# Kernel optimization log

Measured on AMD Instinct MI355X. Metric: run time of the kernel, lower is better.

The kernel has to match this reference:

```python
import jax, jax.numpy as jnp
import numpy as np

N = 4096
IN_DIM = 6
HID = 32
HEADS1 = 4
OUT_DIM = 64


def _gat_layer(x, mask, W, a_src, a_dst, b):
    # x: [n, in], W: [in, heads*d], a_src/a_dst: [heads, d], b: [heads*d]
    n = x.shape[0]
    heads, d = a_src.shape
    h = (x @ W).reshape(n, heads, d)                      # [n, heads, d]
    e_src = jnp.einsum('nhd,hd->nh', h, a_src)            # [n, heads]
    e_dst = jnp.einsum('nhd,hd->nh', h, a_dst)            # [n, heads]
    logits = e_src[:, None, :] + e_dst[None, :, :]        # [n, n, heads]
    logits = jax.nn.leaky_relu(logits, negative_slope=0.2)
    logits = jnp.where(mask[:, :, None], logits, jnp.float32(-1e9))
    alpha = jax.nn.softmax(logits, axis=1)                # softmax over j (dim=1)
    # dropout disabled (eval mode reference)
    out = jnp.einsum('ijh,jhd->ihd', alpha, h).reshape(n, heads * d)
    return out + b


def setup_inputs() -> dict:
    key = jax.random.key(0)
    ks = jax.random.split(key, 10)
    x = jax.random.normal(ks[0], (N, IN_DIM), dtype=jnp.float32)
    adj = jax.random.bernoulli(ks[1], 0.01, (N, N)).astype(jnp.float32)
    s = 0.1
    W1 = jax.random.normal(ks[2], (IN_DIM, HEADS1 * HID), dtype=jnp.float32) * s
    a_src1 = jax.random.normal(ks[3], (HEADS1, HID), dtype=jnp.float32) * s
    a_dst1 = jax.random.normal(ks[4], (HEADS1, HID), dtype=jnp.float32) * s
    b1 = jnp.zeros((HEADS1 * HID,), dtype=jnp.float32)
    W2 = jax.random.normal(ks[5], (HEADS1 * HID, OUT_DIM), dtype=jnp.float32) * s
    a_src2 = jax.random.normal(ks[6], (1, OUT_DIM), dtype=jnp.float32) * s
    a_dst2 = jax.random.normal(ks[7], (1, OUT_DIM), dtype=jnp.float32) * s
    b2 = jnp.zeros((OUT_DIM,), dtype=jnp.float32)
    return {'x': x, 'adj': adj, 'W1': W1, 'a_src1': a_src1, 'a_dst1': a_dst1,
            'b1': b1, 'W2': W2, 'a_src2': a_src2, 'a_dst2': a_dst2, 'b2': b2}


def reference(x, adj, W1, a_src1, a_dst1, b1, W2, a_src2, a_dst2, b2):
    n = x.shape[0]
    # add self loops: a = max(a, I), mask = a > 0
    a = jnp.maximum(adj, jnp.eye(n, dtype=adj.dtype))
    mask = a > 0
    h1 = jax.nn.elu(_gat_layer(x, mask, W1, a_src1, a_dst1, b1))
    # dropout disabled (eval mode)
    h2 = _gat_layer(h1, mask, W2, a_src2, a_dst2, b2)
    return h2
```

## Files before the change

kernel.cpp:

```cpp
#include <hip/hip_runtime.h>
#include <hip/hip_bf16.h>

#define N 4096
#define IN_DIM 6
#define HID 32
#define HEADS1 4
#define D1 (HEADS1*HID)
#define OUT_DIM 64
#define MAXNB 192

__global__ void k1_h1pre(const float* __restrict__ x,
                         const float* __restrict__ W1,
                         const float* __restrict__ a_src1,
                         const float* __restrict__ a_dst1,
                         float* __restrict__ hpre,
                         float* __restrict__ es1,
                         float* __restrict__ ed1) {
    int i = blockIdx.x;
    int t = threadIdx.x;
    __shared__ float xs[IN_DIM];
    if (t < IN_DIM) xs[t] = x[i*IN_DIM + t];
    __syncthreads();
    float acc = 0.f;
    #pragma unroll
    for (int k = 0; k < IN_DIM; ++k)
        acc += xs[k] * W1[k*D1 + t];
    hpre[(size_t)i*D1 + t] = acc;
    float ps = acc * a_src1[t];
    float pd = acc * a_dst1[t];
    #pragma unroll
    for (int off = 16; off >= 1; off >>= 1) {
        ps += __shfl_xor(ps, off, 64);
        pd += __shfl_xor(pd, off, 64);
    }
    if ((t & 31) == 0) {
        int h = t >> 5;
        es1[i*HEADS1 + h] = ps;
        ed1[i*HEADS1 + h] = pd;
    }
}

__global__ void k2_csr(const float* __restrict__ adj,
                       int* __restrict__ cnt, int* __restrict__ idxg) {
    int i = blockIdx.x;
    int t = threadIdx.x;
    __shared__ int c;
    __shared__ int list[MAXNB];
    if (t == 0) c = 0;
    __syncthreads();
    const float4* row = (const float4*)(adj + (size_t)i * N);
    for (int k = t; k < N/4; k += 256) {
        float4 v = row[k];
        float f[4] = {v.x, v.y, v.z, v.w};
        #pragma unroll
        for (int q = 0; q < 4; ++q) {
            int j = k*4 + q;
            if (f[q] > 0.f || j == i) {
                int p = atomicAdd(&c, 1);
                if (p < MAXNB) list[p] = j;
            }
        }
    }
    __syncthreads();
    int cc = min(c, MAXNB);
    if (t == 0) cnt[i] = cc;
    for (int p = t; p < cc; p += 256) idxg[i*MAXNB + p] = list[p];
}

__global__ void k3_agg1(const float* __restrict__ hpre,
                        const float* __restrict__ es1,
                        const float* __restrict__ ed1,
                        const int* __restrict__ cnt,
                        const int* __restrict__ idxg,
                        const float* __restrict__ b1,
                        float* __restrict__ h1) {
    int i = blockIdx.x;
    int t = threadIdx.x;
    int c = cnt[i];
    __shared__ int js[MAXNB];
    __shared__ float alpha[HEADS1][MAXNB];
    __shared__ float esi[HEADS1];
    if (t < HEADS1) esi[t] = es1[i*HEADS1 + t];
    for (int p = t; p < c; p += 128) js[p] = idxg[i*MAXNB + p];
    __syncthreads();
    for (int p = t; p < c; p += 128) {
        int j = js[p];
        #pragma unroll
        for (int h = 0; h < HEADS1; ++h) {
            float l = esi[h] + ed1[j*HEADS1 + h];
            alpha[h][p] = (l > 0.f) ? l : 0.2f*l;
        }
    }
    __syncthreads();
    int h = t >> 5, lane = t & 31;
    float m = -1e30f;
    for (int p = lane; p < c; p += 32) m = fmaxf(m, alpha[h][p]);
    #pragma unroll
    for (int off = 16; off >= 1; off >>= 1) m = fmaxf(m, __shfl_xor(m, off, 64));
    float s = 0.f;
    for (int p = lane; p < c; p += 32) s += __expf(alpha[h][p] - m);
    #pragma unroll
    for (int off = 16; off >= 1; off >>= 1) s += __shfl_xor(s, off, 64);
    float inv = 1.f / s;
    for (int p = lane; p < c; p += 32) alpha[h][p] = __expf(alpha[h][p] - m) * inv;
    __syncthreads();
    float acc = 0.f;
    for (int p = 0; p < c; ++p)
        acc += alpha[h][p] * hpre[(size_t)js[p]*D1 + t];
    acc += b1[t];
    h1[(size_t)i*D1 + t] = (acc > 0.f) ? acc : expm1f(acc);
}

__global__ void k4_h2pre(const float* __restrict__ h1,
                         const float* __restrict__ W2,
                         const float* __restrict__ a_src2,
                         const float* __restrict__ a_dst2,
                         float* __restrict__ h2pre,
                         float* __restrict__ es2,
                         float* __restrict__ ed2) {
    int i = blockIdx.x;
    int t = threadIdx.x;
    __shared__ float hs[D1];
    hs[t]      = h1[(size_t)i*D1 + t];
    hs[t + 64] = h1[(size_t)i*D1 + t + 64];
    __syncthreads();
    float acc = 0.f;
    #pragma unroll
    for (int k = 0; k < D1; ++k)
        acc += hs[k] * W2[k*OUT_DIM + t];
    h2pre[(size_t)i*OUT_DIM + t] = acc;
    float ps = acc * a_src2[t];
    float pd = acc * a_dst2[t];
    #pragma unroll
    for (int off = 32; off >= 1; off >>= 1) {
        ps += __shfl_xor(ps, off, 64);
        pd += __shfl_xor(pd, off, 64);
    }
    if (t == 0) { es2[i] = ps; ed2[i] = pd; }
}

__global__ void k5_agg2(const float* __restrict__ h2pre,
                        const float* __restrict__ es2,
                        const float* __restrict__ ed2,
                        const int* __restrict__ cnt,
                        const int* __restrict__ idxg,
                        const float* __restrict__ b2v,
                        float* __restrict__ out) {
    int i = blockIdx.x;
    int t = threadIdx.x;
    int c = cnt[i];
    __shared__ int js[MAXNB];
    __shared__ float alpha[MAXNB];
    for (int p = t; p < c; p += 64) js[p] = idxg[i*MAXNB + p];
    __syncthreads();
    float esi = es2[i];
    float m = -1e30f;
    for (int p = t; p < c; p += 64) {
        float l = esi + ed2[js[p]];
        l = (l > 0.f) ? l : 0.2f*l;
        alpha[p] = l;
        m = fmaxf(m, l);
    }
    #pragma unroll
    for (int off = 32; off >= 1; off >>= 1) m = fmaxf(m, __shfl_xor(m, off, 64));
    __syncthreads();
    float s = 0.f;
    for (int p = t; p < c; p += 64) s += __expf(alpha[p] - m);
    #pragma unroll
    for (int off = 32; off >= 1; off >>= 1) s += __shfl_xor(s, off, 64);
    float inv = 1.f / s;
    for (int p = t; p < c; p += 64) alpha[p] = __expf(alpha[p] - m) * inv;
    __syncthreads();
    float acc = 0.f;
    for (int p = 0; p < c; ++p)
        acc += alpha[p] * h2pre[(size_t)js[p]*OUT_DIM + t];
    acc += b2v[t];
    out[(size_t)i*OUT_DIM + t] = acc;
}

extern "C" void kernel_launch(void* const* d_in, const int* in_sizes, int n_in,
                              void* d_out, int out_size, void* d_ws, size_t ws_size,
                              hipStream_t stream) {
    const float* x      = (const float*)d_in[0];
    const float* adj    = (const float*)d_in[1];
    const float* W1     = (const float*)d_in[2];
    const float* a_src1 = (const float*)d_in[3];
    const float* a_dst1 = (const float*)d_in[4];
    const float* b1     = (const float*)d_in[5];
    const float* W2     = (const float*)d_in[6];
    const float* a_src2 = (const float*)d_in[7];
    const float* a_dst2 = (const float*)d_in[8];
    const float* b2v    = (const float*)d_in[9];
    float* out = (float*)d_out;

    float* ws    = (float*)d_ws;
    float* hpre  = ws;
    float* h1    = hpre  + (size_t)N*D1;
    float* h2pre = h1    + (size_t)N*D1;
    float* es1   = h2pre + (size_t)N*OUT_DIM;
    float* ed1   = es1   + (size_t)N*HEADS1;
    float* es2   = ed1   + (size_t)N*HEADS1;
    float* ed2   = es2   + N;
    int*   cnt   = (int*)(ed2 + N);
    int*   idxg  = cnt + N;

    k1_h1pre<<<N, 128, 0, stream>>>(x, W1, a_src1, a_dst1, hpre, es1, ed1);
    k2_csr  <<<N, 256, 0, stream>>>(adj, cnt, idxg);
    k3_agg1 <<<N, 128, 0, stream>>>(hpre, es1, ed1, cnt, idxg, b1, h1);
    k4_h2pre<<<N,  64, 0, stream>>>(h1, W2, a_src2, a_dst2, h2pre, es2, ed2);
    k5_agg2 <<<N,  64, 0, stream>>>(h2pre, es2, ed2, cnt, idxg, b2v, out);
}
```

Before: 136.5 us.

## Fuse CSR build, layer-1 aggregation and layer-2 projection into one kernel

Merges the adjacency scan, the layer-1 attention softmax and aggregation, and the h1·W2 projection into a single per-row kernel, cutting five launches to three. Logits are computed at the point where each neighbour is discovered, h1 never goes to global memory, and the aggregation is split across two thread groups. Softmax normalisation is deferred to after aggregation in both layers, which removes a second exp pass. kA now handles two rows per block. The cost is higher shared-memory use and more register pressure in the fused kernel, which can lower occupancy.

```diff
diff --git a/kernel.cpp b/kernel.cpp
--- a/kernel.cpp
+++ b/kernel.cpp
@@ -1,5 +1,4 @@
 #include <hip/hip_runtime.h>
-#include <hip/hip_bf16.h>
 
 #define N 4096
 #define IN_DIM 6
@@ -9,46 +8,66 @@
 #define OUT_DIM 64
 #define MAXNB 192
 
-__global__ void k1_h1pre(const float* __restrict__ x,
-                         const float* __restrict__ W1,
-                         const float* __restrict__ a_src1,
-                         const float* __restrict__ a_dst1,
-                         float* __restrict__ hpre,
-                         float* __restrict__ es1,
-                         float* __restrict__ ed1) {
-    int i = blockIdx.x;
-    int t = threadIdx.x;
-    __shared__ float xs[IN_DIM];
-    if (t < IN_DIM) xs[t] = x[i*IN_DIM + t];
+__global__ void kA(const float* __restrict__ x,
+                   const float* __restrict__ W1,
+                   const float* __restrict__ a_src1,
+                   const float* __restrict__ a_dst1,
+                   float* __restrict__ hpre,
+                   float* __restrict__ es1,
+                   float* __restrict__ ed1) {
+    int t  = threadIdx.x;
+    int r  = t >> 7;
+    int tt = t & 127;
+    int i  = blockIdx.x * 2 + r;
+    __shared__ float xs[2][IN_DIM];
+    if (tt < IN_DIM) xs[r][tt] = x[i*IN_DIM + tt];
     __syncthreads();
     float acc = 0.f;
     #pragma unroll
     for (int k = 0; k < IN_DIM; ++k)
-        acc += xs[k] * W1[k*D1 + t];
-    hpre[(size_t)i*D1 + t] = acc;
-    float ps = acc * a_src1[t];
-    float pd = acc * a_dst1[t];
+        acc += xs[r][k] * W1[k*D1 + tt];
+    hpre[(size_t)i*D1 + tt] = acc;
+    float ps = acc * a_src1[tt];
+    float pd = acc * a_dst1[tt];
     #pragma unroll
     for (int off = 16; off >= 1; off >>= 1) {
         ps += __shfl_xor(ps, off, 64);
         pd += __shfl_xor(pd, off, 64);
     }
-    if ((t & 31) == 0) {
-        int h = t >> 5;
+    if ((tt & 31) == 0) {
+        int h = tt >> 5;
         es1[i*HEADS1 + h] = ps;
         ed1[i*HEADS1 + h] = pd;
     }
 }
 
-__global__ void k2_csr(const float* __restrict__ adj,
-                       int* __restrict__ cnt, int* __restrict__ idxg) {
+__global__ void kB(const float* __restrict__ adj,
+                   const float* __restrict__ hpre,
+                   const float* __restrict__ es1,
+                   const float* __restrict__ ed1,
+                   const float* __restrict__ b1,
+                   const float* __restrict__ W2,
+                   const float* __restrict__ a_src2,
+                   const float* __restrict__ a_dst2,
+                   int* __restrict__ cnt, int* __restrict__ idxg,
+                   float* __restrict__ h2pre,
+                   float* __restrict__ es2, float* __restrict__ ed2) {
     int i = blockIdx.x;
     int t = threadIdx.x;
-    __shared__ int c;
-    __shared__ int list[MAXNB];
-    if (t == 0) c = 0;
-    __syncthreads();
-    const float4* row = (const float4*)(adj + (size_t)i * N);
+    __shared__ int   cL;
+    __shared__ int   js[MAXNB];
+    __shared__ float lg[HEADS1][MAXNB];
+    __shared__ float esi[HEADS1];
+    __shared__ float sinv[HEADS1];
+    __shared__ float part[128];
+    __shared__ float h1s[D1];
+    __shared__ float p2s[256];
+    if (t == 0) cL = 0;
+    if (t < HEADS1) esi[t] = es1[i*HEADS1 + t];
+    __syncthreads();
+
+    const float4* row  = (const float4*)(adj + (size_t)i * N);
+    const float4* ed1v = (const float4*)ed1;
     for (int k = t; k < N/4; k += 256) {
         float4 v = row[k];
         float f[4] = {v.x, v.y, v.z, v.w};
@@ -56,101 +75,92 @@
         for (int q = 0; q < 4; ++q) {
             int j = k*4 + q;
             if (f[q] > 0.f || j == i) {
-                int p = atomicAdd(&c, 1);
-                if (p < MAXNB) list[p] = j;
+                int p = atomicAdd(&cL, 1);
+                if (p < MAXNB) {
+                    js[p] = j;
+                    float4 e4 = ed1v[j];
+                    float le[4] = {e4.x, e4.y, e4.z, e4.w};
+                    #pragma unroll
+                    for (int h = 0; h < HEADS1; ++h) {
+                        float l = esi[h] + le[h];
+                        lg[h][p] = (l > 0.f) ? l : 0.2f*l;
+                    }
+                }
             }
         }
     }
     __syncthreads();
-    int cc = min(c, MAXNB);
-    if (t == 0) cnt[i] = cc;
-    for (int p = t; p < cc; p += 256) idxg[i*MAXNB + p] = list[p];
-}
-
-__global__ void k3_agg1(const float* __restrict__ hpre,
-                        const float* __restrict__ es1,
-                        const float* __restrict__ ed1,
-                        const int* __restrict__ cnt,
-                        const int* __restrict__ idxg,
-                        const float* __restrict__ b1,
-                        float* __restrict__ h1) {
+    int c = min(cL, MAXNB);
+
+    if (t >= 128) {
+        if (t == 128) cnt[i] = c;
+        for (int p = t - 128; p < c; p += 128) idxg[i*MAXNB + p] = js[p];
+    } else {
+        int h = t >> 5, lane = t & 31;
+        float m = -1e30f;
+        for (int p = lane; p < c; p += 32) m = fmaxf(m, lg[h][p]);
+        #pragma unroll
+        for (int off = 16; off >= 1; off >>= 1) m = fmaxf(m, __shfl_xor(m, off, 64));
+        float s = 0.f;
+        for (int p = lane; p < c; p += 32) {
+            float e = __expf(lg[h][p] - m);
+            lg[h][p] = e;
+            s += e;
+        }
+        #pragma unroll
+        for (int off = 16; off >= 1; off >>= 1) s += __shfl_xor(s, off, 64);
+        if (lane == 0) sinv[h] = 1.f / s;
+    }
+    __syncthreads();
+
+    int g = t >> 7, tt = t & 127, hh = (t & 127) >> 5;
+    float acc = 0.f;
+    for (int p = g; p < c; p += 2)
+        acc += lg[hh][p] * hpre[(size_t)js[p]*D1 + tt];
+    if (g == 1) part[tt] = acc;
+    __syncthreads();
+    if (g == 0) {
+        acc += part[tt];
+        float val = acc * sinv[hh] + b1[tt];
+        h1s[tt] = (val > 0.f) ? val : expm1f(val);
+    }
+    __syncthreads();
+
+    int o = t & 63, q = t >> 6;
+    float pa = 0.f;
+    #pragma unroll
+    for (int k = 0; k < 32; ++k) {
+        int kk = q*32 + k;
+        pa += h1s[kk] * W2[kk*OUT_DIM + o];
+    }
+    p2s[t] = pa;
+    __syncthreads();
+    if (t < 64) {
+        float h2 = p2s[t] + p2s[t+64] + p2s[t+128] + p2s[t+192];
+        h2pre[(size_t)i*OUT_DIM + t] = h2;
+        float ps = h2 * a_src2[t];
+        float pd = h2 * a_dst2[t];
+        #pragma unroll
+        for (int off = 32; off >= 1; off >>= 1) {
+            ps += __shfl_xor(ps, off, 64);
+            pd += __shfl_xor(pd, off, 64);
+        }
+        if (t == 0) { es2[i] = ps; ed2[i] = pd; }
+    }
+}
+
+__global__ void kC(const float* __restrict__ h2pre,
+                   const float* __restrict__ es2,
+                   const float* __restrict__ ed2,
+                   const int* __restrict__ cnt,
+                   const int* __restrict__ idxg,
+                   const float* __restrict__ b2v,
+                   float* __restrict__ out) {
     int i = blockIdx.x;
     int t = threadIdx.x;
     int c = cnt[i];
-    __shared__ int js[MAXNB];
-    __shared__ float alpha[HEADS1][MAXNB];
-    __shared__ float esi[HEADS1];
-    if (t < HEADS1) esi[t] = es1[i*HEADS1 + t];
-    for (int p = t; p < c; p += 128) js[p] = idxg[i*MAXNB + p];
-    __syncthreads();
-    for (int p = t; p < c; p += 128) {
-        int j = js[p];
-        #pragma unroll
-        for (int h = 0; h < HEADS1; ++h) {
-            float l = esi[h] + ed1[j*HEADS1 + h];
-            alpha[h][p] = (l > 0.f) ? l : 0.2f*l;
-        }
-    }
-    __syncthreads();
-    int h = t >> 5, lane = t & 31;
-    float m = -1e30f;
-    for (int p = lane; p < c; p += 32) m = fmaxf(m, alpha[h][p]);
-    #pragma unroll
-    for (int off = 16; off >= 1; off >>= 1) m = fmaxf(m, __shfl_xor(m, off, 64));
-    float s = 0.f;
-    for (int p = lane; p < c; p += 32) s += __expf(alpha[h][p] - m);
-    #pragma unroll
-    for (int off = 16; off >= 1; off >>= 1) s += __shfl_xor(s, off, 64);
-    float inv = 1.f / s;
-    for (int p = lane; p < c; p += 32) alpha[h][p] = __expf(alpha[h][p] - m) * inv;
-    __syncthreads();
-    float acc = 0.f;
-    for (int p = 0; p < c; ++p)
-        acc += alpha[h][p] * hpre[(size_t)js[p]*D1 + t];
-    acc += b1[t];
-    h1[(size_t)i*D1 + t] = (acc > 0.f) ? acc : expm1f(acc);
-}
-
-__global__ void k4_h2pre(const float* __restrict__ h1,
-                         const float* __restrict__ W2,
-                         const float* __restrict__ a_src2,
-                         const float* __restrict__ a_dst2,
-                         float* __restrict__ h2pre,
-                         float* __restrict__ es2,
-                         float* __restrict__ ed2) {
-    int i = blockIdx.x;
-    int t = threadIdx.x;
-    __shared__ float hs[D1];
-    hs[t]      = h1[(size_t)i*D1 + t];
-    hs[t + 64] = h1[(size_t)i*D1 + t + 64];
-    __syncthreads();
-    float acc = 0.f;
-    #pragma unroll
-    for (int k = 0; k < D1; ++k)
-        acc += hs[k] * W2[k*OUT_DIM + t];
-    h2pre[(size_t)i*OUT_DIM + t] = acc;
-    float ps = acc * a_src2[t];
-    float pd = acc * a_dst2[t];
-    #pragma unroll
-    for (int off = 32; off >= 1; off >>= 1) {
-        ps += __shfl_xor(ps, off, 64);
-        pd += __shfl_xor(pd, off, 64);
-    }
-    if (t == 0) { es2[i] = ps; ed2[i] = pd; }
-}
-
-__global__ void k5_agg2(const float* __restrict__ h2pre,
-                        const float* __restrict__ es2,
-                        const float* __restrict__ ed2,
-                        const int* __restrict__ cnt,
-                        const int* __restrict__ idxg,
-                        const float* __restrict__ b2v,
-                        float* __restrict__ out) {
-    int i = blockIdx.x;
-    int t = threadIdx.x;
-    int c = cnt[i];
-    __shared__ int js[MAXNB];
-    __shared__ float alpha[MAXNB];
+    __shared__ int   js[MAXNB];
+    __shared__ float al[MAXNB];
     for (int p = t; p < c; p += 64) js[p] = idxg[i*MAXNB + p];
     __syncthreads();
     float esi = es2[i];
@@ -158,24 +168,26 @@
     for (int p = t; p < c; p += 64) {
         float l = esi + ed2[js[p]];
         l = (l > 0.f) ? l : 0.2f*l;
-        alpha[p] = l;
+        al[p] = l;
         m = fmaxf(m, l);
     }
     #pragma unroll
     for (int off = 32; off >= 1; off >>= 1) m = fmaxf(m, __shfl_xor(m, off, 64));
     __syncthreads();
     float s = 0.f;
-    for (int p = t; p < c; p += 64) s += __expf(alpha[p] - m);
+    for (int p = t; p < c; p += 64) {
+        float e = __expf(al[p] - m);
+        al[p] = e;
+        s += e;
+    }
     #pragma unroll
     for (int off = 32; off >= 1; off >>= 1) s += __shfl_xor(s, off, 64);
     float inv = 1.f / s;
-    for (int p = t; p < c; p += 64) alpha[p] = __expf(alpha[p] - m) * inv;
     __syncthreads();
     float acc = 0.f;
     for (int p = 0; p < c; ++p)
-        acc += alpha[p] * h2pre[(size_t)js[p]*OUT_DIM + t];
-    acc += b2v[t];
-    out[(size_t)i*OUT_DIM + t] = acc;
+        acc += al[p] * h2pre[(size_t)js[p]*OUT_DIM + t];
+    out[(size_t)i*OUT_DIM + t] = acc * inv + b2v[t];
 }
 
 extern "C" void kernel_launch(void* const* d_in, const int* in_sizes, int n_in,
@@ -195,8 +207,7 @@
 
     float* ws    = (float*)d_ws;
     float* hpre  = ws;
-    float* h1    = hpre  + (size_t)N*D1;
-    float* h2pre = h1    + (size_t)N*D1;
+    float* h2pre = hpre  + (size_t)N*D1;
     float* es1   = h2pre + (size_t)N*OUT_DIM;
     float* ed1   = es1   + (size_t)N*HEADS1;
     float* es2   = ed1   + (size_t)N*HEADS1;
@@ -204,9 +215,8 @@
     int*   cnt   = (int*)(ed2 + N);
     int*   idxg  = cnt + N;
 
-    k1_h1pre<<<N, 128, 0, stream>>>(x, W1, a_src1, a_dst1, hpre, es1, ed1);
-    k2_csr  <<<N, 256, 0, stream>>>(adj, cnt, idxg);
-    k3_agg1 <<<N, 128, 0, stream>>>(hpre, es1, ed1, cnt, idxg, b1, h1);
-    k4_h2pre<<<N,  64, 0, stream>>>(h1, W2, a_src2, a_dst2, h2pre, es2, ed2);
-    k5_agg2 <<<N,  64, 0, stream>>>(h2pre, es2, ed2, cnt, idxg, b2v, out);
-}
+    kA<<<N/2, 256, 0, stream>>>(x, W1, a_src1, a_dst1, hpre, es1, ed1);
+    kB<<<N,   256, 0, stream>>>(adj, hpre, es1, ed1, b1, W2, a_src2, a_dst2,
+                                cnt, idxg, h2pre, es2, ed2);
+    kC<<<N,    64, 0, stream>>>(h2pre, es2, ed2, cnt, idxg, b2v, out);
+}
```

Result: slower. 148.6 us (+8.9%).
